# Kernel tuning notes

Measured on AMD Instinct MI355X. Metric: run time of the kernel, lower is better.

## Reference

```python
import jax, jax.numpy as jnp
import numpy as np

B, N, T, D = 16, 30, 50, 4
K, H, M, NH = 4, 128, 128, 128
E = N * (N - 1)  # 870


def setup_inputs() -> dict:
    key = jax.random.key(0)
    ks = jax.random.split(key, 12)
    # one-hot receiver / sender matrices for fully connected graph (no self loops)
    pairs = np.array([(i, j) for i in range(N) for j in range(N) if i != j])
    eye = np.eye(N, dtype=np.float32)
    rel_rec = jnp.asarray(eye[pairs[:, 0]])   # [E, N]
    rel_send = jnp.asarray(eye[pairs[:, 1]])  # [E, N]
    s = 0.1
    return {
        "inputs": jax.random.normal(ks[0], (B, N, T, D), jnp.float32),
        "rel_type": jax.random.uniform(ks[1], (B, E, K), jnp.float32),
        "rel_rec": rel_rec,
        "rel_send": rel_send,
        "W1": jax.random.normal(ks[2], (K, 2 * D, H), jnp.float32) * s,
        "b1": jax.random.normal(ks[3], (K, H), jnp.float32) * s,
        "W2": jax.random.normal(ks[4], (K, H, M), jnp.float32) * s,
        "b2": jax.random.normal(ks[5], (K, M), jnp.float32) * s,
        "oW1": jax.random.normal(ks[6], (D + M, NH), jnp.float32) * s,
        "ob1": jax.random.normal(ks[7], (NH,), jnp.float32) * s,
        "oW2": jax.random.normal(ks[8], (NH, NH), jnp.float32) * s,
        "ob2": jax.random.normal(ks[9], (NH,), jnp.float32) * s,
        "oW3": jax.random.normal(ks[10], (NH, D), jnp.float32) * s,
        "ob3": jax.random.normal(ks[11], (D,), jnp.float32) * s,
        "pred_steps": 1,
    }


def _single_step(x, rt, rel_rec, rel_send, W1, b1, W2, b2, oW1, ob1, oW2, ob2, oW3, ob3):
    # x: [B, Ts, N, D], rt: [B, Ts, E, K]
    recv = jnp.einsum('en,btnd->bted', rel_rec, x)
    send = jnp.einsum('en,btnd->bted', rel_send, x)
    pre_msg = jnp.concatenate([recv, send], axis=-1)           # [B,Ts,E,2D]
    all_msgs = jnp.zeros(pre_msg.shape[:-1] + (M,), x.dtype)
    for k in range(K):  # small fixed set of structurally distinct MLPs
        msg = jax.nn.relu(pre_msg @ W1[k] + b1[k])
        msg = jax.nn.relu(msg @ W2[k] + b2[k])
        all_msgs = all_msgs + msg * rt[..., k:k + 1]
    agg = jnp.einsum('btef,en->btnf', all_msgs, rel_rec)       # scatter-sum to receivers
    aug = jnp.concatenate([x, agg], axis=-1)                    # [B,Ts,N,D+M]
    h = jax.nn.relu(aug @ oW1 + ob1)
    h = jax.nn.relu(h @ oW2 + ob2)
    return x + (h @ oW3 + ob3)


def reference(inputs, rel_type, rel_rec, rel_send, W1, b1, W2, b2,
              oW1, ob1, oW2, ob2, oW3, ob3, pred_steps):
    x = jnp.transpose(inputs, (0, 2, 1, 3))                    # [B,T,N,D]
    Tt = x.shape[1]
    rt = jnp.broadcast_to(rel_type[:, None], (rel_type.shape[0], Tt) + rel_type.shape[1:])
    last_pred = x[:, 0::pred_steps]
    curr_rt = rt[:, 0::pred_steps]
    preds = []
    for _ in range(pred_steps):
        last_pred = _single_step(last_pred, curr_rt, rel_rec, rel_send,
                                 W1, b1, W2, b2, oW1, ob1, oW2, ob2, oW3, ob3)
        preds.append(last_pred)
    Ts = preds[0].shape[1]
    out = jnp.stack(preds, axis=2).reshape(x.shape[0], Ts * pred_steps, x.shape[2], x.shape[3])
    pred_all = out[:, :Tt - 1]
    return jnp.transpose(pred_all, (0, 2, 1, 3))               # [B,N,T-1,D]
```

## Files before the change

### kernel.cpp

```cpp
#include <hip/hip_runtime.h>

typedef __bf16 bf16_t;
typedef __bf16 bf16x8 __attribute__((ext_vector_type(8)));
typedef __bf16 bf16x4 __attribute__((ext_vector_type(4)));
typedef float  f32x4  __attribute__((ext_vector_type(4)));

#define NB 16
#define NN 30
#define NT 50
#define ND 4
#define NK 4
#define NE 870

#define C_INPUTS   0
#define C_RELTYPE  96000
#define C_B2       152192
#define C_OB1      152704
#define C_OB2      152832
#define C_OW3      152960
#define C_OB3      153472
#define C_W1F      153480
#define C_W2F      169864
#define C_OW1F     235400
#define C_OW2F     255880
#define AGG_BYTE_OFF (1u << 20)

union U4 { unsigned w[4]; bf16x8 v; };
union U2 { unsigned w[2]; bf16x4 v; };

__device__ __forceinline__ bf16x8 bzero8() {
  bf16x8 z;
#pragma unroll
  for (int j = 0; j < 8; ++j) z[j] = (bf16_t)0.0f;
  return z;
}

__device__ __forceinline__ f32x4 make4(float a, float b, float c, float d) {
  f32x4 v; v[0] = a; v[1] = b; v[2] = c; v[3] = d; return v;
}

__device__ __forceinline__ void pack_store4(bf16_t* dst, f32x4 a) {
  bf16x4 v;
  v[0] = (bf16_t)fmaxf(a[0], 0.0f);
  v[1] = (bf16_t)fmaxf(a[1], 0.0f);
  v[2] = (bf16_t)fmaxf(a[2], 0.0f);
  v[3] = (bf16_t)fmaxf(a[3], 0.0f);
  *(bf16x4*)dst = v;
}

__device__ __forceinline__ void qswap(unsigned x, unsigned y,
                                      unsigned& zlo, unsigned& zhi) {
#if __has_builtin(__builtin_amdgcn_permlane32_swap) && __has_builtin(__builtin_amdgcn_permlane16_swap)
  auto t = __builtin_amdgcn_permlane32_swap(x, y, false, false);
  auto z = __builtin_amdgcn_permlane16_swap(t[0], t[1], false, false);
  zlo = z[0]; zhi = z[1];
#else
  const int lane = threadIdx.x & 63;
  const int quad = lane >> 4;
  const int lm   = lane & 15;
  const int s0 = (((2 * quad) & 3) << 4) + lm;
  const int s1 = (((2 * quad + 1) & 3) << 4) + lm;
  const unsigned a0 = (unsigned)__shfl((int)x, s0, 64);
  const unsigned b0 = (unsigned)__shfl((int)y, s0, 64);
  const unsigned a1 = (unsigned)__shfl((int)x, s1, 64);
  const unsigned b1 = (unsigned)__shfl((int)y, s1, 64);
  zlo = (quad < 2) ? a0 : b0;
  zhi = (quad < 2) ? a1 : b1;
#endif
}

__device__ __forceinline__ int detect_isbf16(const void* p) {
  const unsigned short* w = (const unsigned short*)p;
  int c = 0;
#pragma unroll 4
  for (int i = 0; i < 256; i += 2) {
    const int e = (w[i] >> 7) & 0xFF;
    if (e >= 100 && e <= 150) ++c;
  }
  return c >= 96;
}

__device__ __forceinline__ float ldf(const void* src, int idx, int isbf) {
  return isbf ? (float)((const bf16_t*)src)[idx] : ((const float*)src)[idx];
}

__device__ __forceinline__ void conv_arr(const void* src, bf16_t* dst, int n,
                                         int isbf, int gtid, int gsz) {
  if (isbf) {
    const unsigned short* s = (const unsigned short*)src;
    unsigned short* d = (unsigned short*)dst;
    for (int i = gtid; i < n; i += gsz) d[i] = s[i];
  } else {
    const float* s = (const float*)src;
    for (int i = gtid; i < n; i += gsz) dst[i] = (bf16_t)s[i];
  }
}

__global__ void convert_kernel(const void* inputs, const void* rel_type,
                               const void* W1, const void* b1,
                               const void* W2, const void* b2,
                               const void* oW1, const void* ob1,
                               const void* oW2, const void* ob2,
                               const void* oW3, const void* ob3,
                               void* ws)
{
  __shared__ int sflag;
  if (threadIdx.x == 0) sflag = detect_isbf16(inputs);
  __syncthreads();
  const int isbf = sflag;
  if (blockIdx.x == 0 && threadIdx.x == 0) *(int*)ws = isbf;
  bf16_t* cb = (bf16_t*)((char*)ws + 16);
  const int gtid = blockIdx.x * blockDim.x + threadIdx.x;
  const int gsz  = gridDim.x * blockDim.x;

  conv_arr(inputs,   cb + C_INPUTS,  96000, isbf, gtid, gsz);
  for (int i = gtid; i < 55680; i += gsz) {
    const int bq  = i / (NK * NE);
    const int rem = i - bq * (NK * NE);
    const int k   = rem / NE;
    const int e   = rem - k * NE;
    cb[C_RELTYPE + i] = (bf16_t)ldf(rel_type, (bq * NE + e) * NK + k, isbf);
  }
  conv_arr(b2,  cb + C_B2,  512, isbf, gtid, gsz);
  conv_arr(ob1, cb + C_OB1, 128, isbf, gtid, gsz);
  conv_arr(ob2, cb + C_OB2, 128, isbf, gtid, gsz);
  conv_arr(oW3, cb + C_OW3, 512, isbf, gtid, gsz);
  conv_arr(ob3, cb + C_OB3, 4,   isbf, gtid, gsz);

  for (int i = gtid; i < 16384; i += gsz) {
    const int j = i & 7, lm = (i >> 3) & 15, quad = (i >> 7) & 3;
    const int ct = (i >> 9) & 7, k = (i >> 12) & 3;
    float v = 0.0f;
    if (quad == 0)                 v = ldf(W1, k * 1024 + j * 128 + ct * 16 + lm, isbf);
    else if (quad == 1 && j == 0)  v = ldf(b1, k * 128 + ct * 16 + lm, isbf);
    cb[C_W1F + i] = (bf16_t)v;
  }
  for (int i = gtid; i < 65536; i += gsz) {
    const int j = i & 7;
    const int l64 = (i >> 3) & 63;
    const int ct = (i >> 9) & 7, kc = (i >> 12) & 3, k = (i >> 14) & 3;
    const int quad = l64 >> 4, lm = l64 & 15;
    const int kk = kc * 32 + quad * 8 + j;
    cb[C_W2F + i] = (bf16_t)ldf(W2, k * 16384 + kk * 128 + ct * 16 + lm, isbf);
  }
  for (int i = gtid; i < 20480; i += gsz) {
    const int j = i & 7, lm = (i >> 3) & 15, quad = (i >> 7) & 3;
    const int rem = i >> 9;
    const int kc = rem % 5, ct = rem / 5;
    const int kk = kc * 32 + quad * 8 + j;
    float v = 0.0f;
    if (kk < 132) v = ldf(oW1, kk * 128 + ct * 16 + lm, isbf);
    cb[C_OW1F + i] = (bf16_t)v;
  }
  for (int i = gtid; i < 16384; i += gsz) {
    const int j = i & 7, lm = (i >> 3) & 15, quad = (i >> 7) & 3;
    const int kc = (i >> 9) & 3, ct = (i >> 11) & 7;
    const int kk = kc * 32 + quad * 8 + j;
    cb[C_OW2F + i] = (bf16_t)ldf(oW2, kk * 128 + ct * 16 + lm, isbf);
  }
}

struct EdgeSmem {
  union { bf16_t sfrag[7168]; float aggf[2048]; } u;
  bf16_t xl[128];
};

__global__ __launch_bounds__(256)
__attribute__((amdgpu_waves_per_eu(2, 2)))
void edge_kernel(const bf16_t* __restrict__ inputs,
                 const bf16_t* __restrict__ rtT,
                 const bf16_t* __restrict__ w1f_g,
                 const bf16_t* __restrict__ w2f_g,
                 const bf16_t* __restrict__ b2c,
                 float* __restrict__ aggbuf)
{
  __shared__ EdgeSmem s;
  const int tid   = threadIdx.x;
  const int bid   = blockIdx.x;
  const int nhalf = bid & 1;
  const int bt    = bid >> 1;
  const int b     = bt / NT;
  const int t     = bt - b * NT;
  const int wave  = tid >> 6;
  const int lane  = tid & 63;
  const int quad  = lane >> 4;
  const int lm    = lane & 15;

  if (tid < 30)
    *(uint2*)&s.xl[tid * 4] = *(const uint2*)&inputs[((b * NN + tid) * NT + t) * ND];
  if (tid < 8) s.xl[120 + tid] = (bf16_t)0.0f;

  {
    bf16x4 z; z[0] = z[1] = z[2] = z[3] = (bf16_t)0.0f;
#pragma unroll
    for (int s7 = 0; s7 < 7; ++s7)
      *(bf16x4*)&s.u.sfrag[((s7 * 4 + wave) * 64 + lane) * 4] = z;
  }
  __syncthreads();

  f32x4 aggacc[8];
#pragma unroll
  for (int ct = 0; ct < 8; ++ct) aggacc[ct] = make4(0.f, 0.f, 0.f, 0.f);

#pragma unroll 1
  for (int k = 0; k < NK; ++k) {
    bf16x8 w1r[8];
    bf16x8 w2r[8][4];
    float  b2s[8];
#pragma unroll
    for (int ct = 0; ct < 8; ++ct) {
      w1r[ct] = *(const bf16x8*)&w1f_g[(((k * 8 + ct) * 4 + quad) * 16 + lm) * 8];
#pragma unroll
      for (int kc = 0; kc < 4; ++kc)
        w2r[ct][kc] = *(const bf16x8*)&w2f_g[((((k * 4 + kc) * 8) + ct) * 64 + quad * 16 + lm) * 8];
      b2s[ct] = (float)b2c[k * 128 + ct * 16 + lm];
    }

    {
      const bf16_t* rtk = rtT + (size_t)(b * NK + k) * NE + nhalf * 435;
#pragma unroll
      for (int it = 0; it < 2; ++it) {
        const int idx = it * 64 + lane;
        const int s7  = idx >> 4;
        if (s7 < 7) {
          const int g = s7 * 4 + wave;
          const int i = g * 16 + (idx & 15);
          if (i < 435) {
            const int n    = i / 29;
            const int slot = (g * 64 + ((i >> 2) & 3) * 16 + n) * 4 + (i & 3);
            s.u.sfrag[slot] = rtk[i];
          }
        }
      }
    }

#pragma unroll 1
    for (int tt = 0; tt < 7; ++tt) {
      const int g = tt * 4 + wave;

      bf16x8 pm = bzero8();
      if (quad == 0) {
        const int e    = g * 16 + lm;
        const int d29  = e / 29;
        const int recv = nhalf * 15 + d29;
        const int j29  = e - d29 * 29;
        const int send = j29 + (j29 >= recv);
        union { uint2 u2[2]; bf16x8 v; } c;
        c.u2[0] = *(const uint2*)&s.xl[recv * 4];
        c.u2[1] = *(const uint2*)&s.xl[send * 4];
        if (e < 435) pm = c.v;
      } else if (quad == 1) {
        pm[0] = (bf16_t)1.0f;
      }

      U4 af[4];
      const f32x4 z4 = make4(0.f, 0.f, 0.f, 0.f);
#pragma unroll
      for (int kc = 0; kc < 4; ++kc) {
        f32x4 aA = __builtin_amdgcn_mfma_f32_16x16x32_bf16(w1r[2 * kc],     pm, z4, 0, 0, 0);
        f32x4 aB = __builtin_amdgcn_mfma_f32_16x16x32_bf16(w1r[2 * kc + 1], pm, z4, 0, 0, 0);
        U2 pA, pB;
        pA.v[0] = (bf16_t)fmaxf(aA[0], 0.f); pA.v[1] = (bf16_t)fmaxf(aA[1], 0.f);
        pA.v[2] = (bf16_t)fmaxf(aA[2], 0.f); pA.v[3] = (bf16_t)fmaxf(aA[3], 0.f);
        pB.v[0] = (bf16_t)fmaxf(aB[0], 0.f); pB.v[1] = (bf16_t)fmaxf(aB[1], 0.f);
        pB.v[2] = (bf16_t)fmaxf(aB[2], 0.f); pB.v[3] = (bf16_t)fmaxf(aB[3], 0.f);
        qswap(pA.w[0], pB.w[0], af[kc].w[0], af[kc].w[2]);
        qswap(pA.w[1], pB.w[1], af[kc].w[1], af[kc].w[3]);
      }

      U4 sa;
      {
        U2 s4;
        s4.v = *(const bf16x4*)&s.u.sfrag[(g * 64 + lane) * 4];
        sa.w[0] = s4.w[0]; sa.w[1] = s4.w[1]; sa.w[2] = 0u; sa.w[3] = 0u;
      }

      __builtin_amdgcn_s_setprio(1);
#pragma unroll
      for (int ct = 0; ct < 8; ++ct) {
        f32x4 acc = make4(b2s[ct], b2s[ct], b2s[ct], b2s[ct]);
#pragma unroll
        for (int kc = 0; kc < 4; ++kc)
          acc = __builtin_amdgcn_mfma_f32_16x16x32_bf16(af[kc].v, w2r[ct][kc], acc, 0, 0, 0);
        U4 mb;
        U2 pk;
        pk.v[0] = (bf16_t)fmaxf(acc[0], 0.f); pk.v[1] = (bf16_t)fmaxf(acc[1], 0.f);
        pk.v[2] = (bf16_t)fmaxf(acc[2], 0.f); pk.v[3] = (bf16_t)fmaxf(acc[3], 0.f);
        mb.w[0] = pk.w[0]; mb.w[1] = pk.w[1]; mb.w[2] = 0u; mb.w[3] = 0u;
        aggacc[ct] = __builtin_amdgcn_mfma_f32_16x16x32_bf16(sa.v, mb.v, aggacc[ct], 0, 0, 0);
      }
      __builtin_amdgcn_s_setprio(0);
    }
  }

  __syncthreads();
  for (int i = tid; i < 2048; i += 256) s.u.aggf[i] = 0.0f;
  __syncthreads();
#pragma unroll
  for (int ct = 0; ct < 8; ++ct)
#pragma unroll
    for (int r = 0; r < 4; ++r)
      atomicAdd(&s.u.aggf[(quad * 4 + r) * 128 + ct * 16 + lm], aggacc[ct][r]);
  __syncthreads();
  for (int i = tid; i < 15 * 128; i += 256) {
    const int r = i >> 7, col = i & 127;
    aggbuf[(size_t)(bt * NN + nhalf * 15 + r) * 128 + col] = s.u.aggf[r * 128 + col];
  }
}

struct NodeSmem {
  bf16_t h1[64 * 136];
  bf16_t h2[64 * 136];
  bf16_t xres[64 * 4];
  float  b1f[128];
  float  b2f[128];
  float  w3f[128 * 4];
  float  b3f[4];
};

__global__ __launch_bounds__(256)
void node_kernel(const bf16_t* __restrict__ inputs,
                 const bf16_t* __restrict__ ow1f_g, const bf16_t* __restrict__ ob1,
                 const bf16_t* __restrict__ ow2f_g, const bf16_t* __restrict__ ob2,
                 const bf16_t* __restrict__ oW3, const bf16_t* __restrict__ ob3,
                 const int* __restrict__ flagptr,
                 const float* __restrict__ aggbuf,
                 void* __restrict__ outp)
{
  __shared__ NodeSmem s;
  const int tid  = threadIdx.x;
  const int wave = tid >> 6;
  const int lane = tid & 63;
  const int quad = lane >> 4;
  const int lm   = lane & 15;
  const int row  = wave * 16 + lm;
  const int r0   = blockIdx.x * 64;
  const int isbf = *flagptr;

  if (tid < 64) {
    const int r  = r0 + tid;
    const int n  = r % NN;
    const int bt = r / NN;
    const int t  = bt % NT;
    const int b  = bt / NT;
    *(uint2*)&s.xres[tid * 4] = *(const uint2*)&inputs[((b * NN + n) * NT + t) * ND];
  }
  if (tid < 128) s.b1f[tid] = (float)ob1[tid];
  else           s.b2f[tid - 128] = (float)ob2[tid - 128];
  if (tid < 4) s.b3f[tid] = (float)ob3[tid];
  for (int i = tid; i < 512; i += 256) s.w3f[i] = (float)oW3[i];
  __syncthreads();

  bf16x8 bfa[5];
  {
    const float* aggrow = aggbuf + (size_t)(r0 + row) * 128;
    float tmp[8];
    if (quad == 0) {
#pragma unroll
      for (int j = 0; j < 4; ++j) tmp[j] = (float)s.xres[row * 4 + j];
      const float4 a = *(const float4*)(aggrow);
      tmp[4] = a.x; tmp[5] = a.y; tmp[6] = a.z; tmp[7] = a.w;
    } else {
      const int c0 = quad * 8 - 4;
      const float4 a = *(const float4*)(aggrow + c0);
      const float4 d = *(const float4*)(aggrow + c0 + 4);
      tmp[0] = a.x; tmp[1] = a.y; tmp[2] = a.z; tmp[3] = a.w;
      tmp[4] = d.x; tmp[5] = d.y; tmp[6] = d.z; tmp[7] = d.w;
    }
#pragma unroll
    for (int j = 0; j < 8; ++j) bfa[0][j] = (bf16_t)tmp[j];
#pragma unroll
    for (int kc = 1; kc < 4; ++kc) {
      const int c0 = kc * 32 + quad * 8 - 4;
      const float4 a = *(const float4*)(aggrow + c0);
      const float4 d = *(const float4*)(aggrow + c0 + 4);
      tmp[0] = a.x; tmp[1] = a.y; tmp[2] = a.z; tmp[3] = a.w;
      tmp[4] = d.x; tmp[5] = d.y; tmp[6] = d.z; tmp[7] = d.w;
#pragma unroll
      for (int j = 0; j < 8; ++j) bfa[kc][j] = (bf16_t)tmp[j];
    }
    if (quad == 0) {
      const float4 a = *(const float4*)(aggrow + 124);
      tmp[0] = a.x; tmp[1] = a.y; tmp[2] = a.z; tmp[3] = a.w;
      tmp[4] = 0.f; tmp[5] = 0.f; tmp[6] = 0.f; tmp[7] = 0.f;
#pragma unroll
      for (int j = 0; j < 8; ++j) bfa[4][j] = (bf16_t)tmp[j];
    } else bfa[4] = bzero8();
  }

#pragma unroll
  for (int ct = 0; ct < 8; ++ct) {
    const int nb = ct * 16 + quad * 4;
    f32x4 acc = make4(s.b1f[nb], s.b1f[nb + 1], s.b1f[nb + 2], s.b1f[nb + 3]);
#pragma unroll
    for (int kc = 0; kc < 5; ++kc) {
      const bf16x8 w = *(const bf16x8*)&ow1f_g[(((ct * 5 + kc) * 4 + quad) * 16 + lm) * 8];
      acc = __builtin_amdgcn_mfma_f32_16x16x32_bf16(w, bfa[kc], acc, 0, 0, 0);
    }
    pack_store4(&s.h1[row * 136 + ct * 16 + quad * 4], acc);
  }

  bf16x8 af[4];
#pragma unroll
  for (int kc = 0; kc < 4; ++kc)
    af[kc] = *(const bf16x8*)&s.h1[row * 136 + kc * 32 + quad * 8];

#pragma unroll
  for (int ct = 0; ct < 8; ++ct) {
    const int mb = ct * 16 + quad * 4;
    f32x4 acc = make4(s.b2f[mb], s.b2f[mb + 1], s.b2f[mb + 2], s.b2f[mb + 3]);
#pragma unroll
    for (int kc = 0; kc < 4; ++kc) {
      const bf16x8 w = *(const bf16x8*)&ow2f_g[(((ct * 4 + kc) * 4 + quad) * 16 + lm) * 8];
      acc = __builtin_amdgcn_mfma_f32_16x16x32_bf16(w, af[kc], acc, 0, 0, 0);
    }
    pack_store4(&s.h2[row * 136 + ct * 16 + quad * 4], acc);
  }

  {
    const int rloc = tid >> 2;
    const int d    = tid & 3;
    float a3 = s.b3f[d];
#pragma unroll
    for (int g = 0; g < 16; ++g) {
      const bf16x8 hv = *(const bf16x8*)&s.h2[rloc * 136 + g * 8];
#pragma unroll
      for (int j = 0; j < 8; ++j)
        a3 += (float)hv[j] * s.w3f[(g * 8 + j) * 4 + d];
    }
    a3 += (float)s.xres[rloc * 4 + d];
    const int r  = r0 + rloc;
    const int n  = r % NN;
    const int bt = r / NN;
    const int t  = bt % NT;
    const int b  = bt / NT;
    if (t < NT - 1) {
      const int oidx = ((b * NN + n) * (NT - 1) + t) * ND + d;
      if (isbf) ((bf16_t*)outp)[oidx] = (bf16_t)a3;
      else      ((float*)outp)[oidx]  = a3;
    }
  }
}

extern "C" void kernel_launch(void* const* d_in, const int* in_sizes, int n_in,
                              void* d_out, int out_size, void* d_ws, size_t ws_size,
                              hipStream_t stream) {
  char* ws = (char*)d_ws;
  bf16_t* cb = (bf16_t*)(ws + 16);
  float* aggbuf = (float*)(ws + AGG_BYTE_OFF);

  convert_kernel<<<dim3(256), dim3(256), 0, stream>>>(
      d_in[0], d_in[1], d_in[4], d_in[5], d_in[6], d_in[7],
      d_in[8], d_in[9], d_in[10], d_in[11], d_in[12], d_in[13], d_ws);

  edge_kernel<<<dim3(NB * NT * 2), dim3(256), 0, stream>>>(
      cb + C_INPUTS, cb + C_RELTYPE, cb + C_W1F, cb + C_W2F,
      cb + C_B2, aggbuf);

  node_kernel<<<dim3((NB * NT * NN) / 64), dim3(256), 0, stream>>>(
      cb + C_INPUTS, cb + C_OW1F, cb + C_OB1, cb + C_OW2F, cb + C_OB2,
      cb + C_OW3, cb + C_OB3, (const int*)d_ws, aggbuf, d_out);
}
```

Before: 339.9 us.

## Assign one relation type per wave in edge kernel, build scatter fragment in registers

The edge kernel is reorganised so each wave owns one relation type k and loops over all 28 edge groups. Output columns are processed two tiles at a time to keep fewer W2 fragments live in registers. The per-k shared-memory scatter fragment is replaced by building the receiver-masked rel_type operand in registers from a padded, pre-transposed rel_type layout. Per-wave partial aggregates are merged with shared-memory atomics after each column pair. The waves_per_eu hint is dropped, and the change adds redundant pre-MLP (W1) work per column pair plus more atomics.

Measured after the change: 472.8 us. 1.39x slower.

```diff
diff --git a/kernel.cpp b/kernel.cpp
--- a/kernel.cpp
+++ b/kernel.cpp
@@ -13,7 +13,6 @@
 #define NE 870
 
 #define C_INPUTS   0
-#define C_RELTYPE  96000
 #define C_B2       152192
 #define C_OB1      152704
 #define C_OB2      152832
@@ -23,6 +22,7 @@
 #define C_W2F      169864
 #define C_OW1F     235400
 #define C_OW2F     255880
+#define C_RT2      272264
 #define AGG_BYTE_OFF (1u << 20)
 
 union U4 { unsigned w[4]; bf16x8 v; };
@@ -114,12 +114,16 @@
   const int gsz  = gridDim.x * blockDim.x;
 
   conv_arr(inputs,   cb + C_INPUTS,  96000, isbf, gtid, gsz);
-  for (int i = gtid; i < 55680; i += gsz) {
-    const int bq  = i / (NK * NE);
-    const int rem = i - bq * (NK * NE);
-    const int k   = rem / NE;
-    const int e   = rem - k * NE;
-    cb[C_RELTYPE + i] = (bf16_t)ldf(rel_type, (bq * NE + e) * NK + k, isbf);
+  for (int i = gtid; i < 57344; i += gsz) {
+    const int eh   = i % 448;
+    const int q    = i / 448;
+    const int half = q & 1;
+    const int k    = (q >> 1) & 3;
+    const int bq   = q >> 3;
+    float v = 0.0f;
+    if (eh < 435)
+      v = ldf(rel_type, (bq * NE + half * 435 + eh) * NK + k, isbf);
+    cb[C_RT2 + i] = (bf16_t)v;
   }
   conv_arr(b2,  cb + C_B2,  512, isbf, gtid, gsz);
   conv_arr(ob1, cb + C_OB1, 128, isbf, gtid, gsz);
@@ -161,12 +165,11 @@
 }
 
 struct EdgeSmem {
-  union { bf16_t sfrag[7168]; float aggf[2048]; } u;
+  float  aggf[2048];
   bf16_t xl[128];
 };
 
 __global__ __launch_bounds__(256)
-__attribute__((amdgpu_waves_per_eu(2, 2)))
 void edge_kernel(const bf16_t* __restrict__ inputs,
                  const bf16_t* __restrict__ rtT,
                  const bf16_t* __restrict__ w1f_g,
@@ -185,70 +188,52 @@
   const int lane  = tid & 63;
   const int quad  = lane >> 4;
   const int lm    = lane & 15;
+  const int k     = wave;
 
   if (tid < 30)
     *(uint2*)&s.xl[tid * 4] = *(const uint2*)&inputs[((b * NN + tid) * NT + t) * ND];
   if (tid < 8) s.xl[120 + tid] = (bf16_t)0.0f;
-
-  {
-    bf16x4 z; z[0] = z[1] = z[2] = z[3] = (bf16_t)0.0f;
-#pragma unroll
-    for (int s7 = 0; s7 < 7; ++s7)
-      *(bf16x4*)&s.u.sfrag[((s7 * 4 + wave) * 64 + lane) * 4] = z;
-  }
+  for (int i = tid; i < 2048; i += 256) s.aggf[i] = 0.0f;
   __syncthreads();
 
-  f32x4 aggacc[8];
-#pragma unroll
-  for (int ct = 0; ct < 8; ++ct) aggacc[ct] = make4(0.f, 0.f, 0.f, 0.f);
+  const bf16_t* rtk = rtT + (size_t)((b * NK + k) * 2 + nhalf) * 448;
+  bf16x8 w1r[8];
+#pragma unroll
+  for (int ct = 0; ct < 8; ++ct)
+    w1r[ct] = *(const bf16x8*)&w1f_g[(((k * 8 + ct) * 4 + quad) * 16 + lm) * 8];
 
 #pragma unroll 1
-  for (int k = 0; k < NK; ++k) {
-    bf16x8 w1r[8];
-    bf16x8 w2r[8][4];
-    float  b2s[8];
-#pragma unroll
-    for (int ct = 0; ct < 8; ++ct) {
-      w1r[ct] = *(const bf16x8*)&w1f_g[(((k * 8 + ct) * 4 + quad) * 16 + lm) * 8];
+  for (int p = 0; p < 4; ++p) {
+    bf16x8 w2r[2][4];
+    float  b2s[2];
+#pragma unroll
+    for (int c = 0; c < 2; ++c) {
+      const int ct = 2 * p + c;
 #pragma unroll
       for (int kc = 0; kc < 4; ++kc)
-        w2r[ct][kc] = *(const bf16x8*)&w2f_g[((((k * 4 + kc) * 8) + ct) * 64 + quad * 16 + lm) * 8];
-      b2s[ct] = (float)b2c[k * 128 + ct * 16 + lm];
-    }
-
-    {
-      const bf16_t* rtk = rtT + (size_t)(b * NK + k) * NE + nhalf * 435;
-#pragma unroll
-      for (int it = 0; it < 2; ++it) {
-        const int idx = it * 64 + lane;
-        const int s7  = idx >> 4;
-        if (s7 < 7) {
-          const int g = s7 * 4 + wave;
-          const int i = g * 16 + (idx & 15);
-          if (i < 435) {
-            const int n    = i / 29;
-            const int slot = (g * 64 + ((i >> 2) & 3) * 16 + n) * 4 + (i & 3);
-            s.u.sfrag[slot] = rtk[i];
-          }
-        }
-      }
-    }
+        w2r[c][kc] = *(const bf16x8*)&w2f_g[((((k * 4 + kc) * 8) + ct) * 64 + quad * 16 + lm) * 8];
+      b2s[c] = (float)b2c[k * 128 + ct * 16 + lm];
+    }
+    f32x4 agac[2];
+    agac[0] = make4(0.f, 0.f, 0.f, 0.f);
+    agac[1] = make4(0.f, 0.f, 0.f, 0.f);
 
 #pragma unroll 1
-    for (int tt = 0; tt < 7; ++tt) {
-      const int g = tt * 4 + wave;
+    for (int g = 0; g < 28; ++g) {
+      U2 rt4;
+      rt4.v = *(const bf16x4*)&rtk[g * 16 + quad * 4];
 
       bf16x8 pm = bzero8();
       if (quad == 0) {
         const int e    = g * 16 + lm;
-        const int d29  = e / 29;
+        const int d29  = (e * 565) >> 14;
         const int recv = nhalf * 15 + d29;
         const int j29  = e - d29 * 29;
         const int send = j29 + (j29 >= recv);
-        union { uint2 u2[2]; bf16x8 v; } c;
-        c.u2[0] = *(const uint2*)&s.xl[recv * 4];
-        c.u2[1] = *(const uint2*)&s.xl[send * 4];
-        if (e < 435) pm = c.v;
+        union { uint2 u2[2]; bf16x8 v; } cc;
+        cc.u2[0] = *(const uint2*)&s.xl[recv * 4];
+        cc.u2[1] = *(const uint2*)&s.xl[send * 4];
+        if (e < 435) pm = cc.v;
       } else if (quad == 1) {
         pm[0] = (bf16_t)1.0f;
       }
@@ -270,41 +255,47 @@
 
       U4 sa;
       {
-        U2 s4;
-        s4.v = *(const bf16x4*)&s.u.sfrag[(g * 64 + lane) * 4];
-        sa.w[0] = s4.w[0]; sa.w[1] = s4.w[1]; sa.w[2] = 0u; sa.w[3] = 0u;
+        bf16x4 sv;
+#pragma unroll
+        for (int j = 0; j < 4; ++j) {
+          const int ej  = g * 16 + quad * 4 + j;
+          const int d29 = (ej * 565) >> 14;
+          sv[j] = (d29 == lm) ? rt4.v[j] : (bf16_t)0.0f;
+        }
+        U2 sw; sw.v = sv;
+        sa.w[0] = sw.w[0]; sa.w[1] = sw.w[1]; sa.w[2] = 0u; sa.w[3] = 0u;
       }
 
       __builtin_amdgcn_s_setprio(1);
 #pragma unroll
-      for (int ct = 0; ct < 8; ++ct) {
-        f32x4 acc = make4(b2s[ct], b2s[ct], b2s[ct], b2s[ct]);
+      for (int c = 0; c < 2; ++c) {
+        f32x4 acc = make4(b2s[c], b2s[c], b2s[c], b2s[c]);
 #pragma unroll
         for (int kc = 0; kc < 4; ++kc)
-          acc = __builtin_amdgcn_mfma_f32_16x16x32_bf16(af[kc].v, w2r[ct][kc], acc, 0, 0, 0);
+          acc = __builtin_amdgcn_mfma_f32_16x16x32_bf16(af[kc].v, w2r[c][kc], acc, 0, 0, 0);
         U4 mb;
         U2 pk;
         pk.v[0] = (bf16_t)fmaxf(acc[0], 0.f); pk.v[1] = (bf16_t)fmaxf(acc[1], 0.f);
         pk.v[2] = (bf16_t)fmaxf(acc[2], 0.f); pk.v[3] = (bf16_t)fmaxf(acc[3], 0.f);
         mb.w[0] = pk.w[0]; mb.w[1] = pk.w[1]; mb.w[2] = 0u; mb.w[3] = 0u;
-        aggacc[ct] = __builtin_amdgcn_mfma_f32_16x16x32_bf16(sa.v, mb.v, aggacc[ct], 0, 0, 0);
+        agac[c] = __builtin_amdgcn_mfma_f32_16x16x32_bf16(sa.v, mb.v, agac[c], 0, 0, 0);
       }
       __builtin_amdgcn_s_setprio(0);
     }
-  }
-
-  __syncthreads();
-  for (int i = tid; i < 2048; i += 256) s.u.aggf[i] = 0.0f;
-  __syncthreads();
-#pragma unroll
-  for (int ct = 0; ct < 8; ++ct)
-#pragma unroll
-    for (int r = 0; r < 4; ++r)
-      atomicAdd(&s.u.aggf[(quad * 4 + r) * 128 + ct * 16 + lm], aggacc[ct][r]);
+
+#pragma unroll
+    for (int c = 0; c < 2; ++c) {
+      const int ct = 2 * p + c;
+#pragma unroll
+      for (int r = 0; r < 4; ++r)
+        atomicAdd(&s.aggf[(quad * 4 + r) * 128 + ct * 16 + lm], agac[c][r]);
+    }
+  }
+
   __syncthreads();
   for (int i = tid; i < 15 * 128; i += 256) {
     const int r = i >> 7, col = i & 127;
-    aggbuf[(size_t)(bt * NN + nhalf * 15 + r) * 128 + col] = s.u.aggf[r * 128 + col];
+    aggbuf[(size_t)(bt * NN + nhalf * 15 + r) * 128 + col] = s.aggf[r * 128 + col];
   }
 }
 
@@ -454,7 +445,7 @@
       d_in[8], d_in[9], d_in[10], d_in[11], d_in[12], d_in[13], d_ws);
 
   edge_kernel<<<dim3(NB * NT * 2), dim3(256), 0, stream>>>(
-      cb + C_INPUTS, cb + C_RELTYPE, cb + C_W1F, cb + C_W2F,
+      cb + C_INPUTS, cb + C_RT2, cb + C_W1F, cb + C_W2F,
       cb + C_B2, aggbuf);
 
   node_kernel<<<dim3((NB * NT * NN) / 64), dim3(256), 0, stream>>>(
```
